# Kernel tuning notes

Hardware: AMD Instinct MI355X
Metric: run time of the kernel (lower is better)

The kernel has to match this reference:

```python
import jax, jax.numpy as jnp
from jax import lax
import numpy as np

B, T, V, H = 64, 256, 4096, 512


def setup_inputs() -> dict:
    key = jax.random.key(0)
    k1, k2, k3, k4 = jax.random.split(key, 4)
    x = jax.random.randint(k1, (B, T), 0, V, dtype=jnp.int32)
    # RNNScratch params (std=0.01 normal init, as in the LM head)
    Wxh = 0.01 * jax.random.normal(k2, (V, H), dtype=jnp.float32)
    Whh = 0.01 * jax.random.normal(k3, (H, H), dtype=jnp.float32)
    bh = jnp.zeros((H,), dtype=jnp.float32)
    Wo = 0.01 * jax.random.normal(k4, (H, V), dtype=jnp.float32)
    Bo = jnp.zeros((V,), dtype=jnp.float32)
    return {"x": x, "Wxh": Wxh, "Whh": Whh, "bh": bh, "Wo": Wo, "Bo": Bo}


def reference(x, Wxh, Whh, bh, Wo, Bo):
    # one_hot(x).float() @ Wxh is exactly a row gather from Wxh
    xs = jnp.take(Wxh, x.T, axis=0)  # [T, B, H]
    h0 = jnp.zeros((x.shape[0], Whh.shape[0]), dtype=Wxh.dtype)

    def step(h, xt):
        h = jnp.tanh(xt + h @ Whh + bh)  # [B, H]
        return h, h

    _, hs = lax.scan(step, h0, xs)  # hs: [T, B, H]
    # per-step output projection, fused into one einsum over time
    out = jnp.einsum("tbh,hv->btv", hs, Wo) + Bo  # [B, T, V]
    return out
```

## Files before the change

kernel.cpp:

```cpp
#include <hip/hip_runtime.h>


typedef __fp16 half2_t __attribute__((ext_vector_type(2)));
typedef __attribute__((ext_vector_type(8))) short short8;
typedef __attribute__((ext_vector_type(4))) float f32x4;

__device__ __forceinline__ unsigned short f32_to_bf16(float f) {
  unsigned int u = __builtin_bit_cast(unsigned int, f);
  u = (u + 0x7FFFu + ((u >> 16) & 1u)) >> 16;
  return (unsigned short)u;
}

__device__ __forceinline__ unsigned int pack_f16x2(float a, float b) {
  half2_t h = __builtin_amdgcn_cvt_pkrtz(a, b);
  return __builtin_bit_cast(unsigned int, h);
}

__device__ __forceinline__ float fdot2_(unsigned int w, unsigned int h, float acc) {
  return __builtin_amdgcn_fdot2(__builtin_bit_cast(half2_t, w),
                                __builtin_bit_cast(half2_t, h), acc, false);
}

__device__ __forceinline__ void glds16(const void* g, void* lds) {
  __builtin_amdgcn_global_load_lds(
      (const __attribute__((address_space(1))) unsigned int*)g,
      (__attribute__((address_space(3))) unsigned int*)lds, 16, 0, 0);
}

__global__ __launch_bounds__(256) void pack_whhB(const float* __restrict__ Whh,
                                                 unsigned int* __restrict__ WhhB,
                                                 unsigned long long* __restrict__ hG64) {
  int idx = blockIdx.x * 256 + threadIdx.x;
  int e = idx & 3;
  int G = idx >> 2;
  int c = G & 127;
  int u = (G >> 7) & 15;
  int q = (G >> 11) & 3;
  int s = G >> 13;
  int p = q * 64 + u * 4 + e;
  int j = s * 128 + c;
  float f0 = Whh[(2 * p) * 512 + j];
  float f1 = Whh[(2 * p + 1) * 512 + j];
  WhhB[idx] = pack_f16x2(f0, f1);
  if (idx < 32768) hG64[idx] = 0ull;
}

__global__ __launch_bounds__(256) void transpose_wo(const float* __restrict__ Wo,
                                                    unsigned short* __restrict__ WoT) {
  __shared__ float tile[64][65];
  const int tv = blockIdx.x;
  const int th = blockIdx.y;
  const int tid = threadIdx.x;
  const int c = tid & 63, r4 = tid >> 6;
#pragma unroll
  for (int p = 0; p < 16; ++p) {
    int hl = p * 4 + r4;
    tile[hl][c] = Wo[(size_t)(th * 64 + hl) * 4096 + tv * 64 + c];
  }
  __syncthreads();
#pragma unroll
  for (int p = 0; p < 16; ++p) {
    int vl = p * 4 + r4;
    WoT[(size_t)(tv * 64 + vl) * 512 + th * 64 + c] = f32_to_bf16(tile[c][vl]);
  }
}

#define DOTU(u_, A) do { \
  const uint4 w_ = wlds[(q16 + (u_)) * 128 + c]; \
  const uint4 h_ = hbuf[q16 + (u_)]; \
  A = fdot2_(w_.x, h_.x, A); A = fdot2_(w_.y, h_.y, A); \
  A = fdot2_(w_.z, h_.z, A); A = fdot2_(w_.w, h_.w, A); } while (0)

__global__ __launch_bounds__(512) void rnn_scanB(const int* __restrict__ x,
                                                 const float* __restrict__ Wxh,
                                                 const unsigned int* __restrict__ WhhB,
                                                 const float* __restrict__ bh,
                                                 unsigned short* __restrict__ hs,
                                                 unsigned long long* hG64) {
  __shared__ uint4 wlds[8192];
  __shared__ uint4 hbuf[64];
  __shared__ float pbuf[512];
  __shared__ int toks[256];
  const int bid = blockIdx.x;
  const int s = bid & 3;
  const int b = bid >> 2;
  const int tid = threadIdx.x;
  const int c = tid & 127;
  const int q = tid >> 7;
  const int q16 = q * 16;
  const uint4* W4 = (const uint4*)WhhB;

#pragma unroll
  for (int it = 0; it < 16; ++it) {
    int L = it * 512 + tid;
    wlds[L] = W4[s * 8192 + L];
  }
  if (tid < 64) hbuf[tid] = make_uint4(0u, 0u, 0u, 0u);
  if (tid < 256) toks[tid] = x[b * 256 + tid];
  __syncthreads();

  unsigned int* hb32 = (unsigned int*)hbuf;
  const float2* Wxh2 = (const float2*)Wxh;
  const float2* bh2 = (const float2*)bh;
  const float2 bhv = (tid < 64) ? bh2[64 * s + tid] : make_float2(0.f, 0.f);

  for (int t = 0; t < 256; ++t) {
    const int tok = toks[t];
    if (t > 0) {
      if (tid < 192) {
        const int r = (tid < s * 64) ? tid : tid + 64;
        const unsigned long long* src =
            hG64 + (((size_t)(t & 1)) << 14) + b * 256 + r;
        unsigned long long v;
        do {
          v = __hip_atomic_load(src, __ATOMIC_RELAXED, __HIP_MEMORY_SCOPE_AGENT);
        } while ((unsigned)(v >> 32) != (unsigned)t);
        hb32[r] = (unsigned)v;
      }
      __syncthreads();
    }

    float a0 = 0.f, a1 = 0.f, a2 = 0.f, a3 = 0.f;
    DOTU(0, a0);  DOTU(1, a1);  DOTU(2, a2);  DOTU(3, a3);
    DOTU(4, a0);  DOTU(5, a1);  DOTU(6, a2);  DOTU(7, a3);
    DOTU(8, a0);  DOTU(9, a1);  DOTU(10, a2); DOTU(11, a3);
    DOTU(12, a0); DOTU(13, a1); DOTU(14, a2); DOTU(15, a3);
    pbuf[q * 128 + c] = (a0 + a1) + (a2 + a3);
    __syncthreads();

    if (tid < 64) {
      const int f = tid;
      const float s1 = pbuf[2 * f] + pbuf[128 + 2 * f] + pbuf[256 + 2 * f] + pbuf[384 + 2 * f];
      const float s2 = pbuf[2 * f + 1] + pbuf[128 + 2 * f + 1] + pbuf[256 + 2 * f + 1] + pbuf[384 + 2 * f + 1];
      const float2 xv = Wxh2[(size_t)tok * 256 + 64 * s + f];
      const float h1 = tanhf(xv.x + s1 + bhv.x);
      const float h2 = tanhf(xv.y + s2 + bhv.y);
      const unsigned int hp = pack_f16x2(h1, h2);
      __hip_atomic_store(hG64 + (((size_t)((t + 1) & 1)) << 14) + b * 256 + 64 * s + f,
                         ((unsigned long long)(unsigned)(t + 1) << 32) | hp,
                         __ATOMIC_RELAXED, __HIP_MEMORY_SCOPE_AGENT);
      hb32[64 * s + f] = hp;
      unsigned int bb = (unsigned int)f32_to_bf16(h1) |
                        ((unsigned int)f32_to_bf16(h2) << 16);
      ((unsigned int*)hs)[(size_t)(b * 256 + t) * 256 + 64 * s + f] = bb;
    }
    __syncthreads();
  }
}

__global__ __launch_bounds__(256) void gemm_out(const unsigned short* __restrict__ A,
                                                const unsigned short* __restrict__ Bt,
                                                const float* __restrict__ Bo,
                                                float* __restrict__ C) {
  __shared__ alignas(16) unsigned short As[128 * 32];
  __shared__ alignas(16) unsigned short Bs[128 * 32];
  const int tid = threadIdx.x;
  const int lane = tid & 63, wid = tid >> 6;
  const int bn = blockIdx.x & 31, bm = blockIdx.x >> 5;
  const int wr = wid >> 1, wc = wid & 1;

  f32x4 acc[4][4] = {};

  const unsigned short* Ag = A + (size_t)(bm * 128 + (tid >> 2)) * 512 + (tid & 3) * 8;
  const unsigned short* Bg = Bt + (size_t)(bn * 128 + (tid >> 2)) * 512 + (tid & 3) * 8;
  char* AsW = (char*)As + wid * 1024;
  char* BsW = (char*)Bs + wid * 1024;

  const int laneRow = lane & 15;
  const int k0 = (lane >> 4) * 8;

  for (int kt = 0; kt < 16; ++kt) {
    __syncthreads();
    const unsigned short* a0 = Ag + kt * 32;
    const unsigned short* b0 = Bg + kt * 32;
    glds16(a0,            AsW);
    glds16(a0 + 64 * 512, AsW + 4096);
    glds16(b0,            BsW);
    glds16(b0 + 64 * 512, BsW + 4096);
    __syncthreads();

    short8 af[4], bf[4];
#pragma unroll
    for (int f = 0; f < 4; ++f)
      af[f] = *(const short8*)&As[(wr * 64 + f * 16 + laneRow) * 32 + k0];
#pragma unroll
    for (int f = 0; f < 4; ++f)
      bf[f] = *(const short8*)&Bs[(wc * 64 + f * 16 + laneRow) * 32 + k0];
#pragma unroll
    for (int fm = 0; fm < 4; ++fm)
#pragma unroll
      for (int fn = 0; fn < 4; ++fn)
        acc[fm][fn] = __builtin_amdgcn_mfma_f32_16x16x32_bf16(af[fm], bf[fn], acc[fm][fn], 0, 0, 0);
  }

  const int mg0 = bm * 128 + wr * 64, ng0 = bn * 128 + wc * 64;
#pragma unroll
  for (int fn = 0; fn < 4; ++fn) {
    const int col = ng0 + fn * 16 + laneRow;
    const float bo = Bo[col];
#pragma unroll
    for (int fm = 0; fm < 4; ++fm) {
      const int row0 = mg0 + fm * 16 + (lane >> 4) * 4;
#pragma unroll
      for (int r = 0; r < 4; ++r)
        C[(size_t)(row0 + r) * 4096 + col] = acc[fm][fn][r] + bo;
    }
  }
}

extern "C" void kernel_launch(void* const* d_in, const int* in_sizes, int n_in,
                              void* d_out, int out_size, void* d_ws, size_t ws_size,
                              hipStream_t stream) {
  (void)in_sizes; (void)n_in; (void)out_size; (void)ws_size;
  const int* x = (const int*)d_in[0];
  const float* Wxh = (const float*)d_in[1];
  const float* Whh = (const float*)d_in[2];
  const float* bh = (const float*)d_in[3];
  const float* Wo = (const float*)d_in[4];
  const float* Bo = (const float*)d_in[5];
  float* out = (float*)d_out;

  unsigned int* WhhB = (unsigned int*)d_ws;
  unsigned short* WoT = (unsigned short*)((char*)d_ws + 524288);
  unsigned short* hs = (unsigned short*)((char*)d_ws + 4718592);
  unsigned long long* hG64 = (unsigned long long*)((char*)d_ws + 21495808);

  hipLaunchKernelGGL(pack_whhB, dim3(512), dim3(256), 0, stream, Whh, WhhB, hG64);
  hipLaunchKernelGGL(transpose_wo, dim3(64, 8), dim3(256), 0, stream, Wo, WoT);
  hipLaunchKernelGGL(rnn_scanB, dim3(256), dim3(512), 0, stream, x, Wxh, WhhB, bh,
                     hs, hG64);
  hipLaunchKernelGGL(gemm_out, dim3(4096), dim3(256), 0, stream, hs, WoT, Bo, out);
}
```

Baseline: 544.4 us.

## Overlap local-slice matvec with cross-block hidden-state polling in RNN scan

The recurrent matvec is reordered so each block first accumulates the contribution from its own locally produced hidden slice, then polls the other blocks' slices and finishes the remaining three quarters. The goal is to hide part of the inter-block synchronization latency behind useful compute. Blocks now publish the pre-activation values, and consumers apply tanh after reading, which takes tanh off the producer's critical path before the store. The Wxh gather is issued early and the final reduction is spread over 128 threads. The cost is redundant tanh work on the consumer side and a changed rounding order, since the pre-activation is stored in fp16 before tanh.

Result: faster. 518.0 us, median of 2 (-4.8%).

```diff
diff --git a/kernel.cpp b/kernel.cpp
--- a/kernel.cpp
+++ b/kernel.cpp
@@ -65,13 +65,13 @@
   }
 }
 
-#define DOTU(u_, A) do { \
-  const uint4 w_ = wlds[(q16 + (u_)) * 128 + c]; \
-  const uint4 h_ = hbuf[q16 + (u_)]; \
+#define DOTK(kc_, A) do { \
+  const uint4 w_ = wlds[(kc_) * 128 + c]; \
+  const uint4 h_ = hbuf[(kc_)]; \
   A = fdot2_(w_.x, h_.x, A); A = fdot2_(w_.y, h_.y, A); \
   A = fdot2_(w_.z, h_.z, A); A = fdot2_(w_.w, h_.w, A); } while (0)
 
-__global__ __launch_bounds__(512) void rnn_scanB(const int* __restrict__ x,
+__global__ __launch_bounds__(512) void rnn_scanD(const int* __restrict__ x,
                                                  const float* __restrict__ Wxh,
                                                  const unsigned int* __restrict__ WhhB,
                                                  const float* __restrict__ bh,
@@ -87,7 +87,7 @@
   const int tid = threadIdx.x;
   const int c = tid & 127;
   const int q = tid >> 7;
-  const int q16 = q * 16;
+  const int s16 = s * 16;
   const uint4* W4 = (const uint4*)WhhB;
 
 #pragma unroll
@@ -100,49 +100,60 @@
   __syncthreads();
 
   unsigned int* hb32 = (unsigned int*)hbuf;
-  const float2* Wxh2 = (const float2*)Wxh;
-  const float2* bh2 = (const float2*)bh;
-  const float2 bhv = (tid < 64) ? bh2[64 * s + tid] : make_float2(0.f, 0.f);
+  const float bhj = (tid < 128) ? bh[s * 128 + tid] : 0.f;
 
   for (int t = 0; t < 256; ++t) {
     const int tok = toks[t];
-    if (t > 0) {
-      if (tid < 192) {
-        const int r = (tid < s * 64) ? tid : tid + 64;
-        const unsigned long long* src =
-            hG64 + (((size_t)(t & 1)) << 14) + b * 256 + r;
-        unsigned long long v;
-        do {
-          v = __hip_atomic_load(src, __ATOMIC_RELAXED, __HIP_MEMORY_SCOPE_AGENT);
-        } while ((unsigned)(v >> 32) != (unsigned)t);
-        hb32[r] = (unsigned)v;
+    const float xv = (tid < 128) ? Wxh[(size_t)tok * 512 + s * 128 + tid] : 0.f;
+
+    float a0 = 0.f, a1 = 0.f, a2 = 0.f, a3 = 0.f;
+    DOTK(s16 + 0 + q, a0); DOTK(s16 + 4 + q, a1);
+    DOTK(s16 + 8 + q, a2); DOTK(s16 + 12 + q, a3);
+
+    if (t > 0 && tid < 192) {
+      const int r = (tid < s * 64) ? tid : tid + 64;
+      const unsigned long long* src =
+          hG64 + (((size_t)(t & 1)) << 14) + b * 256 + r;
+      unsigned long long v;
+      do {
+        v = __hip_atomic_load(src, __ATOMIC_RELAXED, __HIP_MEMORY_SCOPE_AGENT);
+      } while ((unsigned)(v >> 32) != (unsigned)t);
+      half2_t up = __builtin_bit_cast(half2_t, (unsigned)v);
+      hb32[r] = pack_f16x2(tanhf((float)up.x), tanhf((float)up.y));
+    }
+    __syncthreads();
+
+    {
+      int m1 = ((s + 1) & 3) * 16;
+      DOTK(m1 + 0 + q, a0); DOTK(m1 + 4 + q, a1);
+      DOTK(m1 + 8 + q, a2); DOTK(m1 + 12 + q, a3);
+      int m2 = ((s + 2) & 3) * 16;
+      DOTK(m2 + 0 + q, a0); DOTK(m2 + 4 + q, a1);
+      DOTK(m2 + 8 + q, a2); DOTK(m2 + 12 + q, a3);
+      int m3 = ((s + 3) & 3) * 16;
+      DOTK(m3 + 0 + q, a0); DOTK(m3 + 4 + q, a1);
+      DOTK(m3 + 8 + q, a2); DOTK(m3 + 12 + q, a3);
+    }
+    pbuf[q * 128 + c] = (a0 + a1) + (a2 + a3);
+    __syncthreads();
+
+    if (tid < 128) {
+      const float ssum = pbuf[tid] + pbuf[tid + 128] + pbuf[tid + 256] + pbuf[tid + 384];
+      const float u1 = xv + ssum + bhj;
+      const float u2 = __shfl_down(u1, 1);
+      if (!(tid & 1)) {
+        const unsigned int up = pack_f16x2(u1, u2);
+        __hip_atomic_store(
+            hG64 + (((size_t)((t + 1) & 1)) << 14) + b * 256 + 64 * s + (tid >> 1),
+            ((unsigned long long)(unsigned)(t + 1) << 32) | up,
+            __ATOMIC_RELAXED, __HIP_MEMORY_SCOPE_AGENT);
+        half2_t uo = __builtin_bit_cast(half2_t, up);
+        const float h1 = tanhf((float)uo.x);
+        const float h2 = tanhf((float)uo.y);
+        hb32[64 * s + (tid >> 1)] = pack_f16x2(h1, h2);
+        ((unsigned int*)hs)[(size_t)(b * 256 + t) * 256 + 64 * s + (tid >> 1)] =
+            (unsigned int)f32_to_bf16(h1) | ((unsigned int)f32_to_bf16(h2) << 16);
       }
-      __syncthreads();
-    }
-
-    float a0 = 0.f, a1 = 0.f, a2 = 0.f, a3 = 0.f;
-    DOTU(0, a0);  DOTU(1, a1);  DOTU(2, a2);  DOTU(3, a3);
-    DOTU(4, a0);  DOTU(5, a1);  DOTU(6, a2);  DOTU(7, a3);
-    DOTU(8, a0);  DOTU(9, a1);  DOTU(10, a2); DOTU(11, a3);
-    DOTU(12, a0); DOTU(13, a1); DOTU(14, a2); DOTU(15, a3);
-    pbuf[q * 128 + c] = (a0 + a1) + (a2 + a3);
-    __syncthreads();
-
-    if (tid < 64) {
-      const int f = tid;
-      const float s1 = pbuf[2 * f] + pbuf[128 + 2 * f] + pbuf[256 + 2 * f] + pbuf[384 + 2 * f];
-      const float s2 = pbuf[2 * f + 1] + pbuf[128 + 2 * f + 1] + pbuf[256 + 2 * f + 1] + pbuf[384 + 2 * f + 1];
-      const float2 xv = Wxh2[(size_t)tok * 256 + 64 * s + f];
-      const float h1 = tanhf(xv.x + s1 + bhv.x);
-      const float h2 = tanhf(xv.y + s2 + bhv.y);
-      const unsigned int hp = pack_f16x2(h1, h2);
-      __hip_atomic_store(hG64 + (((size_t)((t + 1) & 1)) << 14) + b * 256 + 64 * s + f,
-                         ((unsigned long long)(unsigned)(t + 1) << 32) | hp,
-                         __ATOMIC_RELAXED, __HIP_MEMORY_SCOPE_AGENT);
-      hb32[64 * s + f] = hp;
-      unsigned int bb = (unsigned int)f32_to_bf16(h1) |
-                        ((unsigned int)f32_to_bf16(h2) << 16);
-      ((unsigned int*)hs)[(size_t)(b * 256 + t) * 256 + 64 * s + f] = bb;
     }
     __syncthreads();
   }
@@ -227,7 +238,7 @@
 
   hipLaunchKernelGGL(pack_whhB, dim3(512), dim3(256), 0, stream, Whh, WhhB, hG64);
   hipLaunchKernelGGL(transpose_wo, dim3(64, 8), dim3(256), 0, stream, Wo, WoT);
-  hipLaunchKernelGGL(rnn_scanB, dim3(256), dim3(512), 0, stream, x, Wxh, WhhB, bh,
+  hipLaunchKernelGGL(rnn_scanD, dim3(256), dim3(512), 0, stream, x, Wxh, WhhB, bh,
                      hs, hG64);
   hipLaunchKernelGGL(gemm_out, dim3(4096), dim3(256), 0, stream, hs, WoT, Bo, out);
 }
```
